# Kernel tuning notes

Measured on AMD Instinct MI355X. Metric: run time of the kernel, lower is better.

Reference implementation:

```python
import jax, jax.numpy as jnp
import numpy as np

DIM = 64  # head dim, init arg
SCALE = DIM ** -0.5

def setup_inputs() -> dict:
    key = jax.random.key(0)
    kq, kk, kv = jax.random.split(key, 3)
    shape = (4, 2048, 8, 64)  # (b, n, h, d)
    q = jax.random.normal(kq, shape, dtype=jnp.float32)
    k = jax.random.normal(kk, shape, dtype=jnp.float32)
    v = jax.random.normal(kv, shape, dtype=jnp.float32)
    return {"q": q, "k": k, "v": v}

def reference(q, k, v):
    # score: [b, h, n_q, n_k] -- matches torch bmm over (b*h) batched [n, d] x [d, n]
    score = jnp.einsum('bqhd,bkhd->bhqk', q, k) * SCALE
    attn = jax.nn.softmax(score, axis=-1)
    # context back to [b, n, h, d] (torch permutes h,b,n,d -> b,n,h,d)
    context = jnp.einsum('bhqk,bkhd->bqhd', attn, v)
    return context
```

## Files before the change

kernel.cpp:

```cpp
#include <hip/hip_runtime.h>

#define B 4
#define N 2048
#define H 8
#define D 64
#define HD 512
#define PLS 72

typedef _Float16 half8 __attribute__((ext_vector_type(8)));
typedef _Float16 half4 __attribute__((ext_vector_type(4)));
typedef float float4_ __attribute__((ext_vector_type(4)));

__global__ void prep_kernel(const float* __restrict__ K, const float* __restrict__ V,
                            _Float16* __restrict__ Kf, _Float16* __restrict__ Vtr) {
    __shared__ _Float16 tile[64][PLS];
    const int t = threadIdx.x;
    if (blockIdx.x < 2048) {
        const size_t i = (size_t)blockIdx.x * 256 + t;
        const float4_* p = (const float4_*)(K + i * 8);
        float4_ a = p[0], b = p[1];
        half8 hh;
        #pragma unroll
        for (int j = 0; j < 4; ++j) { hh[j] = (_Float16)a[j]; hh[4 + j] = (_Float16)b[j]; }
        *(half8*)(Kf + i * 8) = hh;
    } else {
        const int bid = blockIdx.x - 2048;
        const int nt = bid & 31, h = (bid >> 5) & 7, b = bid >> 8;
        {
            const int i = t >> 2, c0 = (t & 3) * 16;
            const float* vp = V + (size_t)b * N * HD + (size_t)(nt * 64 + i) * HD + h * D + c0;
            #pragma unroll
            for (int j = 0; j < 4; ++j) {
                float4_ a = *(const float4_*)(vp + j * 4);
                #pragma unroll
                for (int c = 0; c < 4; ++c) tile[i][c0 + j * 4 + c] = (_Float16)a[c];
            }
        }
        __syncthreads();
        {
            const int d = t >> 2, n0 = (t & 3) * 16;
            half8 lo, hi;
            #pragma unroll
            for (int j = 0; j < 8; ++j) { lo[j] = tile[n0 + j][d]; hi[j] = tile[n0 + 8 + j][d]; }
            _Float16* op = Vtr + ((size_t)(b * H + h) * D + d) * N + nt * 64 + n0;
            *(half8*)op = lo;
            *(half8*)(op + 8) = hi;
        }
    }
}

__device__ __forceinline__ void stage_k(const _Float16* __restrict__ Kbh, int keybase,
                                        _Float16* kb, int wave, int lane) {
    const int rsub = lane >> 3, slot = lane & 7;
    #pragma unroll
    for (int i = 0; i < 2; ++i) {
        const int row = wave * 16 + i * 8 + rsub;
        const int c = slot ^ (row & 7);
        __builtin_amdgcn_global_load_lds(
            (const __attribute__((address_space(1))) void*)(Kbh + (size_t)(keybase + row) * HD + c * 8),
            (__attribute__((address_space(3))) void*)(kb + (wave * 16 + i * 8) * 64), 16, 0, 0);
    }
}
__device__ __forceinline__ void stage_v(const _Float16* __restrict__ Vbh, int keybase,
                                        _Float16* vb, int wave, int lane) {
    const int rsub = lane >> 3, slot = lane & 7;
    #pragma unroll
    for (int i = 0; i < 2; ++i) {
        const int row = wave * 16 + i * 8 + rsub;
        const int c = slot ^ (row & 7);
        __builtin_amdgcn_global_load_lds(
            (const __attribute__((address_space(1))) void*)(Vbh + (size_t)row * N + keybase + c * 8),
            (__attribute__((address_space(3))) void*)(vb + (wave * 16 + i * 8) * 64), 16, 0, 0);
    }
}

__device__ __forceinline__ void do_st4(const _Float16* Kt, const half8 qf[4][2],
                                       float lsum[4], _Float16* PwW, int m, int quad) {
    half8 kfr[4][2];
    #pragma unroll
    for (int blk = 0; blk < 4; ++blk) {
        const int key = blk * 16 + m;
        kfr[blk][0] = *(const half8*)(Kt + key * 64 + ((quad ^ (m & 7)) * 8));
        kfr[blk][1] = *(const half8*)(Kt + key * 64 + (((4 + quad) ^ (m & 7)) * 8));
    }
    #pragma unroll
    for (int blk = 0; blk < 4; ++blk) {
        #pragma unroll
        for (int u = 0; u < 4; ++u) {
            float4_ acc = {};
            acc = __builtin_amdgcn_mfma_f32_16x16x32_f16(kfr[blk][0], qf[u][0], acc, 0, 0, 0);
            acc = __builtin_amdgcn_mfma_f32_16x16x32_f16(kfr[blk][1], qf[u][1], acc, 0, 0, 0);
            half4 pk;
            #pragma unroll
            for (int r = 0; r < 4; ++r) {
                float p = __builtin_amdgcn_exp2f(acc[r]);
                lsum[u] += p;
                pk[r] = (_Float16)p;
            }
            *(half4*)(PwW + (u * 16 + m) * 64 + ((blk * 16 + quad * 4) ^ ((m & 7) << 3))) = pk;
        }
    }
}

__device__ __forceinline__ void load_af4(half8 af[4][2], const _Float16* PwW, int m, int quad) {
    #pragma unroll
    for (int u = 0; u < 4; ++u)
        #pragma unroll
        for (int ks = 0; ks < 2; ++ks)
            af[u][ks] = *(const half8*)(PwW + (u * 16 + m) * 64
                                        + ((ks * 32 + quad * 8) ^ ((m & 7) << 3)));
}

__device__ __forceinline__ void do_pv4(const _Float16* Vtile, const half8 af[4][2],
                                       float4_ o[4][4], int m, int quad) {
    #pragma unroll
    for (int ks = 0; ks < 2; ++ks)
        #pragma unroll
        for (int db = 0; db < 4; ++db) {
            half8 bf = *(const half8*)(Vtile + (db * 16 + m) * 64
                                       + ((((ks << 2) + quad) ^ (m & 7)) * 8));
            #pragma unroll
            for (int u = 0; u < 4; ++u)
                o[u][db] = __builtin_amdgcn_mfma_f32_16x16x32_f16(af[u][ks], bf, o[u][db], 0, 0, 0);
        }
}

__global__ __launch_bounds__(256, 2)
void fattn6_kernel(const float* __restrict__ Q, const _Float16* __restrict__ Kf,
                   const _Float16* __restrict__ Vt, float* __restrict__ O0,
                   float* __restrict__ O1, float* __restrict__ L0, float* __restrict__ L1)
{
    __shared__ __align__(16) _Float16 Kb[2][64 * 64];
    __shared__ __align__(16) _Float16 Vb[2][64 * 64];
    __shared__ __align__(16) _Float16 Pw[4][64 * 64];

    const int tid  = threadIdx.x;
    const int wave = tid >> 6;
    const int lane = tid & 63;
    const int m    = lane & 15;
    const int quad = lane >> 4;

    const int s  = blockIdx.x & 1;
    const int qt = blockIdx.x >> 1;
    const int h  = blockIdx.y;
    const int b  = blockIdx.z;
    const int q_base = qt * 256 + wave * 64;
    const int kofs = s * (N / 2);
    const int NIT = (N / 2) / 64;

    const size_t bh_q = (size_t)b * N * HD + (size_t)h * D;
    const _Float16* Kbh = Kf + bh_q;
    const _Float16* Vbh = Vt + (size_t)(b * H + h) * D * N;
    _Float16* PwW = Pw[wave];

    const float SC = 0.125f * 1.4426950408889634f;
    half8 qf[4][2];
    #pragma unroll
    for (int u = 0; u < 4; ++u) {
        const float* qp = Q + bh_q + (size_t)(q_base + u * 16 + m) * HD + quad * 8;
        float4_ a0 = *(const float4_*)qp,        a1 = *(const float4_*)(qp + 4);
        float4_ b0 = *(const float4_*)(qp + 32), b1 = *(const float4_*)(qp + 36);
        #pragma unroll
        for (int jj = 0; jj < 4; ++jj) {
            qf[u][0][jj] = (_Float16)(a0[jj] * SC); qf[u][0][4 + jj] = (_Float16)(a1[jj] * SC);
            qf[u][1][jj] = (_Float16)(b0[jj] * SC); qf[u][1][4 + jj] = (_Float16)(b1[jj] * SC);
        }
    }

    float4_ o[4][4] = {};
    float lsum[4] = {0.f, 0.f, 0.f, 0.f};

    stage_k(Kbh, kofs, Kb[0], wave, lane);
    __syncthreads();
    stage_k(Kbh, kofs + 64, Kb[1], wave, lane);
    stage_v(Vbh, kofs, Vb[0], wave, lane);
    do_st4(Kb[0], qf, lsum, PwW, m, quad);

    for (int t = 1; t < NIT; ++t) {
        __syncthreads();
        if (t + 1 < NIT)
            stage_k(Kbh, kofs + (t + 1) * 64, Kb[(t + 1) & 1], wave, lane);
        stage_v(Vbh, kofs + t * 64, Vb[t & 1], wave, lane);

        half8 af[4][2];
        load_af4(af, PwW, m, quad);
        do_st4(Kb[t & 1], qf, lsum, PwW, m, quad);
        do_pv4(Vb[(t - 1) & 1], af, o, m, quad);
    }

    __syncthreads();
    {
        half8 af[4][2];
        load_af4(af, PwW, m, quad);
        do_pv4(Vb[(NIT - 1) & 1], af, o, m, quad);
    }

    float lr[4];
    #pragma unroll
    for (int u = 0; u < 4; ++u) {
        float v = lsum[u];
        v += __shfl_xor(v, 16, 64);
        v += __shfl_xor(v, 32, 64);
        lr[u] = v;
    }
    float* Od = s ? O1 : O0;
    float* Ld = s ? L1 : L0;
    if (lane < 16) {
        #pragma unroll
        for (int u = 0; u < 4; ++u)
            Ld[(size_t)(b * H + h) * N + q_base + u * 16 + lane] = lr[u];
    }
    #pragma unroll
    for (int u = 0; u < 4; ++u)
        #pragma unroll
        for (int db = 0; db < 4; ++db)
            #pragma unroll
            for (int r = 0; r < 4; ++r) {
                const int row = q_base + u * 16 + quad * 4 + r;
                Od[bh_q + (size_t)row * HD + db * 16 + m] = o[u][db][r];
            }
}

__global__ void combine_kernel(float* __restrict__ out, const float* __restrict__ O1,
                               const float* __restrict__ L0, const float* __restrict__ L1) {
    const size_t i = ((size_t)blockIdx.x * 256 + threadIdx.x) * 4;
    const int hh = (int)((i >> 6) & 7);
    const int nn = (int)((i >> 9) & 2047);
    const int bb = (int)(i >> 20);
    const size_t qi = ((size_t)(bb * 8 + hh) << 11) | (size_t)nn;
    const float r = 1.0f / (L0[qi] + L1[qi]);
    float4_ a = *(const float4_*)(out + i);
    float4_ c = *(const float4_*)(O1 + i);
    float4_ res;
    #pragma unroll
    for (int j = 0; j < 4; ++j) res[j] = (a[j] + c[j]) * r;
    *(float4_*)(out + i) = res;
}

__device__ __forceinline__ void do_st(const _Float16* Kt, const half8 qf[2][2],
                                      float lsum[2], _Float16* PwW, int m, int quad) {
    #pragma unroll
    for (int blk = 0; blk < 4; ++blk) {
        const int key = blk * 16 + m;
        half8 kf0 = *(const half8*)(Kt + key * 64 + ((quad ^ (m & 7)) * 8));
        half8 kf1 = *(const half8*)(Kt + key * 64 + (((4 + quad) ^ (m & 7)) * 8));
        #pragma unroll
        for (int u = 0; u < 2; ++u) {
            float4_ acc = {};
            acc = __builtin_amdgcn_mfma_f32_16x16x32_f16(kf0, qf[u][0], acc, 0, 0, 0);
            acc = __builtin_amdgcn_mfma_f32_16x16x32_f16(kf1, qf[u][1], acc, 0, 0, 0);
            half4 pk;
            #pragma unroll
            for (int r = 0; r < 4; ++r) {
                float p = __builtin_amdgcn_exp2f(acc[r]);
                lsum[u] += p;
                pk[r] = (_Float16)p;
            }
            *(half4*)(PwW + (u * 16 + m) * 64 + ((blk * 16 + quad * 4) ^ ((m & 7) << 3))) = pk;
        }
    }
}
__device__ __forceinline__ void load_af(half8 af[2][2], const _Float16* PwW, int m, int quad) {
    #pragma unroll
    for (int u = 0; u < 2; ++u)
        #pragma unroll
        for (int ks = 0; ks < 2; ++ks)
            af[u][ks] = *(const half8*)(PwW + (u * 16 + m) * 64
                                        + ((ks * 32 + quad * 8) ^ ((m & 7) << 3)));
}
__device__ __forceinline__ void do_pv(const _Float16* Vtile, const half8 af[2][2],
                                      float4_ o[2][4], int m, int quad) {
    #pragma unroll
    for (int ks = 0; ks < 2; ++ks)
        #pragma unroll
        for (int db = 0; db < 4; ++db) {
            half8 bf = *(const half8*)(Vtile + (db * 16 + m) * 64
                                       + ((((ks << 2) + quad) ^ (m & 7)) * 8));
            #pragma unroll
            for (int u = 0; u < 2; ++u)
                o[u][db] = __builtin_amdgcn_mfma_f32_16x16x32_f16(af[u][ks], bf, o[u][db], 0, 0, 0);
        }
}

__global__ __launch_bounds__(256, 2)
void fattn5_kernel(const float* __restrict__ Q, const _Float16* __restrict__ Kf,
                   const _Float16* __restrict__ Vt, float* __restrict__ Out)
{
    __shared__ __align__(16) _Float16 Kb[2][64 * 64];
    __shared__ __align__(16) _Float16 Vb[2][64 * 64];
    __shared__ __align__(16) _Float16 Pw[4][32 * 64];

    const int tid  = threadIdx.x;
    const int wave = tid >> 6, lane = tid & 63;
    const int m = lane & 15, quad = lane >> 4;
    const int h = blockIdx.y, b = blockIdx.z;
    const int q_base = blockIdx.x * 128 + wave * 32;
    const size_t bh_q = (size_t)b * N * HD + (size_t)h * D;
    const _Float16* Kbh = Kf + bh_q;
    const _Float16* Vbh = Vt + (size_t)(b * H + h) * D * N;
    _Float16* PwW = Pw[wave];
    const float SC = 0.125f * 1.4426950408889634f;
    half8 qf[2][2];
    #pragma unroll
    for (int u = 0; u < 2; ++u) {
        const float* qp = Q + bh_q + (size_t)(q_base + u * 16 + m) * HD + quad * 8;
        float4_ a0 = *(const float4_*)qp,        a1 = *(const float4_*)(qp + 4);
        float4_ b0 = *(const float4_*)(qp + 32), b1 = *(const float4_*)(qp + 36);
        #pragma unroll
        for (int jj = 0; jj < 4; ++jj) {
            qf[u][0][jj] = (_Float16)(a0[jj] * SC); qf[u][0][4 + jj] = (_Float16)(a1[jj] * SC);
            qf[u][1][jj] = (_Float16)(b0[jj] * SC); qf[u][1][4 + jj] = (_Float16)(b1[jj] * SC);
        }
    }
    float4_ o[2][4] = {};
    float lsum[2] = {0.f, 0.f};
    stage_k(Kbh, 0, Kb[0], wave, lane);
    __syncthreads();
    stage_k(Kbh, 64, Kb[1], wave, lane);
    stage_v(Vbh, 0, Vb[0], wave, lane);
    do_st(Kb[0], qf, lsum, PwW, m, quad);
    for (int t = 1; t < 32; ++t) {
        __syncthreads();
        if (t + 1 < 32) stage_k(Kbh, (t + 1) * 64, Kb[(t + 1) & 1], wave, lane);
        stage_v(Vbh, t * 64, Vb[t & 1], wave, lane);
        half8 af[2][2];
        load_af(af, PwW, m, quad);
        do_st(Kb[t & 1], qf, lsum, PwW, m, quad);
        do_pv(Vb[(t - 1) & 1], af, o, m, quad);
    }
    __syncthreads();
    {
        half8 af[2][2];
        load_af(af, PwW, m, quad);
        do_pv(Vb[31 & 1], af, o, m, quad);
    }
    float inv[2];
    #pragma unroll
    for (int u = 0; u < 2; ++u) {
        float v = lsum[u];
        v += __shfl_xor(v, 16, 64);
        v += __shfl_xor(v, 32, 64);
        inv[u] = 1.0f / v;
    }
    #pragma unroll
    for (int u = 0; u < 2; ++u)
        #pragma unroll
        for (int r = 0; r < 4; ++r) {
            const int src = (lane & 48) | (quad * 4 + r);
            const float linv = __shfl(inv[u], src, 64);
            const int row = q_base + u * 16 + quad * 4 + r;
            #pragma unroll
            for (int db = 0; db < 4; ++db)
                Out[bh_q + (size_t)row * HD + db * 16 + m] = o[u][db][r] * linv;
        }
}

__global__ __launch_bounds__(256, 2)
void fattn_fb_kernel(const float* __restrict__ Q, const float* __restrict__ K,
                     const float* __restrict__ V, float* __restrict__ Out)
{
    __shared__ __align__(16) _Float16 Ks[64][PLS];
    __shared__ __align__(16) _Float16 Vts[D][PLS];
    __shared__ __align__(16) _Float16 Pwf[4][16][PLS];
    const int tid = threadIdx.x, wave = tid >> 6, lane = tid & 63;
    const int m = lane & 15, quad = lane >> 4;
    const int q_base = blockIdx.x * 64;
    const size_t bh_off = ((size_t)blockIdx.z * N * H + (size_t)blockIdx.y) * D;
    const float SCALE = 0.125f;
    const int qrow = q_base + wave * 16 + m;
    const float* qp = Q + bh_off + (size_t)qrow * HD + quad * 8;
    half8 qf0, qf1;
    #pragma unroll
    for (int j = 0; j < 8; ++j) qf0[j] = (_Float16)(qp[j] * SCALE);
    #pragma unroll
    for (int j = 0; j < 8; ++j) qf1[j] = (_Float16)(qp[32 + j] * SCALE);
    float4_ o[4] = {};
    float mi[4], li[4];
    #pragma unroll
    for (int r = 0; r < 4; ++r) { mi[r] = -1e30f; li[r] = 0.0f; }
    for (int kt = 0; kt < N; kt += 64) {
        __syncthreads();
        {
            const int key = tid >> 2, c0 = (tid & 3) * 16;
            const float* kp = K + bh_off + (size_t)(kt + key) * HD + c0;
            half8 lo, hi;
            #pragma unroll
            for (int j = 0; j < 8; ++j) lo[j] = (_Float16)kp[j];
            #pragma unroll
            for (int j = 0; j < 8; ++j) hi[j] = (_Float16)kp[8 + j];
            *(half8*)&Ks[key][c0] = lo;
            *(half8*)&Ks[key][c0 + 8] = hi;
        }
        {
            const int c0 = (tid & 15) * 4, k0 = (tid >> 4) * 4;
            const float* vp = V + bh_off + (size_t)(kt + k0) * HD + c0;
            #pragma unroll
            for (int c = 0; c < 4; ++c)
                #pragma unroll
                for (int i = 0; i < 4; ++i)
                    Vts[c0 + c][k0 + i] = (_Float16)vp[i * HD + c];
        }
        __syncthreads();
        float4_ s[4];
        #pragma unroll
        for (int blk = 0; blk < 4; ++blk) {
            const int key = blk * 16 + m;
            half8 kf0 = *(const half8*)&Ks[key][quad * 8];
            half8 kf1 = *(const half8*)&Ks[key][32 + quad * 8];
            float4_ acc = {};
            acc = __builtin_amdgcn_mfma_f32_16x16x32_f16(qf0, kf0, acc, 0, 0, 0);
            acc = __builtin_amdgcn_mfma_f32_16x16x32_f16(qf1, kf1, acc, 0, 0, 0);
            s[blk] = acc;
        }
        float alpha[4];
        #pragma unroll
        for (int r = 0; r < 4; ++r) {
            float v0 = fmaxf(fmaxf(s[0][r], s[1][r]), fmaxf(s[2][r], s[3][r]));
            #pragma unroll
            for (int mask = 1; mask < 16; mask <<= 1) v0 = fmaxf(v0, __shfl_xor(v0, mask, 64));
            float mn = fmaxf(mi[r], v0);
            alpha[r] = __expf(mi[r] - mn);
            mi[r] = mn;
        }
        #pragma unroll
        for (int blk = 0; blk < 4; ++blk)
            #pragma unroll
            for (int r = 0; r < 4; ++r) s[blk][r] = __expf(s[blk][r] - mi[r]);
        #pragma unroll
        for (int r = 0; r < 4; ++r) {
            float tt = s[0][r] + s[1][r] + s[2][r] + s[3][r];
            #pragma unroll
            for (int mask = 1; mask < 16; mask <<= 1) tt += __shfl_xor(tt, mask, 64);
            li[r] = li[r] * alpha[r] + tt;
        }
        #pragma unroll
        for (int d = 0; d < 4; ++d)
            #pragma unroll
            for (int r = 0; r < 4; ++r) o[d][r] *= alpha[r];
        #pragma unroll
        for (int blk = 0; blk < 4; ++blk)
            #pragma unroll
            for (int r = 0; r < 4; ++r)
                Pwf[wave][quad * 4 + r][blk * 16 + m] = (_Float16)s[blk][r];
        #pragma unroll
        for (int ks = 0; ks < 2; ++ks) {
            half8 af = *(const half8*)&Pwf[wave][m][ks * 32 + quad * 8];
            #pragma unroll
            for (int d = 0; d < 4; ++d) {
                half8 bf = *(const half8*)&Vts[d * 16 + m][ks * 32 + quad * 8];
                o[d] = __builtin_amdgcn_mfma_f32_16x16x32_f16(af, bf, o[d], 0, 0, 0);
            }
        }
    }
    #pragma unroll
    for (int d = 0; d < 4; ++d)
        #pragma unroll
        for (int r = 0; r < 4; ++r) {
            const int row = q_base + wave * 16 + quad * 4 + r;
            Out[bh_off + (size_t)row * HD + d * 16 + m] = o[d][r] / li[r];
        }
}

extern "C" void kernel_launch(void* const* d_in, const int* in_sizes, int n_in,
                              void* d_out, int out_size, void* d_ws, size_t ws_size,
                              hipStream_t stream) {
    const float* q = (const float*)d_in[0];
    const float* k = (const float*)d_in[1];
    const float* v = (const float*)d_in[2];
    float* out = (float*)d_out;

    const size_t nelem = (size_t)B * N * H * D;
    const size_t nrows = (size_t)B * H * N;
    const size_t need5 = 2 * nelem * sizeof(_Float16);
    const size_t need6 = need5 + nelem * sizeof(float) + 2 * nrows * sizeof(float);

    if (ws_size >= need6) {
        _Float16* Kf  = (_Float16*)d_ws;
        _Float16* Vtr = Kf + nelem;
        float* O1 = (float*)(Vtr + nelem);
        float* L0 = O1 + nelem;
        float* L1 = L0 + nrows;
        prep_kernel<<<dim3(3072), 256, 0, stream>>>(k, v, Kf, Vtr);
        fattn6_kernel<<<dim3(16, H, B), 256, 0, stream>>>(q, Kf, Vtr, out, O1, L0, L1);
        combine_kernel<<<dim3(4096), 256, 0, stream>>>(out, O1, L0, L1);
    } else if (ws_size >= need5) {
        _Float16* Kf  = (_Float16*)d_ws;
        _Float16* Vtr = Kf + nelem;
        prep_kernel<<<dim3(3072), 256, 0, stream>>>(k, v, Kf, Vtr);
        fattn5_kernel<<<dim3(16, H, B), 256, 0, stream>>>(q, Kf, Vtr, out);
    } else {
        fattn_fb_kernel<<<dim3(N / 64, H, B), 256, 0, stream>>>(q, k, v, out);
    }
}
```

Before: 144.2 us.

## Split keys four ways with fp16 partials and single-buffered smaller LDS

Raises the key-dimension split from two to four, so the attention grid has twice as many blocks. LDS use drops from double-buffered K/V plus 64-wide P to single buffers plus a 32-wide P tile, and launch bounds move to four blocks per CU. Partial outputs are now stored in fp16 and reduced across four splits by a new combine kernel. This targets higher occupancy and better CU fill, at the cost of losing the load/compute overlap of double buffering, adding two barriers per iteration, more combine traffic, and fp16 rounding of the partial sums.

Result: slower. 352.9 us (+144.7%).

```diff
diff --git a/kernel.cpp b/kernel.cpp
--- a/kernel.cpp
+++ b/kernel.cpp
@@ -6,6 +6,9 @@
 #define D 64
 #define HD 512
 #define PLS 72
+#define NELEM ((size_t)B * N * H * D)
+#define NROWS ((size_t)B * H * N)
+#define SPLIT 4
 
 typedef _Float16 half8 __attribute__((ext_vector_type(8)));
 typedef _Float16 half4 __attribute__((ext_vector_type(4)));
@@ -74,65 +77,14 @@
     }
 }
 
-__device__ __forceinline__ void do_st4(const _Float16* Kt, const half8 qf[4][2],
-                                       float lsum[4], _Float16* PwW, int m, int quad) {
-    half8 kfr[4][2];
-    #pragma unroll
-    for (int blk = 0; blk < 4; ++blk) {
-        const int key = blk * 16 + m;
-        kfr[blk][0] = *(const half8*)(Kt + key * 64 + ((quad ^ (m & 7)) * 8));
-        kfr[blk][1] = *(const half8*)(Kt + key * 64 + (((4 + quad) ^ (m & 7)) * 8));
-    }
-    #pragma unroll
-    for (int blk = 0; blk < 4; ++blk) {
-        #pragma unroll
-        for (int u = 0; u < 4; ++u) {
-            float4_ acc = {};
-            acc = __builtin_amdgcn_mfma_f32_16x16x32_f16(kfr[blk][0], qf[u][0], acc, 0, 0, 0);
-            acc = __builtin_amdgcn_mfma_f32_16x16x32_f16(kfr[blk][1], qf[u][1], acc, 0, 0, 0);
-            half4 pk;
-            #pragma unroll
-            for (int r = 0; r < 4; ++r) {
-                float p = __builtin_amdgcn_exp2f(acc[r]);
-                lsum[u] += p;
-                pk[r] = (_Float16)p;
-            }
-            *(half4*)(PwW + (u * 16 + m) * 64 + ((blk * 16 + quad * 4) ^ ((m & 7) << 3))) = pk;
-        }
-    }
-}
-
-__device__ __forceinline__ void load_af4(half8 af[4][2], const _Float16* PwW, int m, int quad) {
-    #pragma unroll
-    for (int u = 0; u < 4; ++u)
-        #pragma unroll
-        for (int ks = 0; ks < 2; ++ks)
-            af[u][ks] = *(const half8*)(PwW + (u * 16 + m) * 64
-                                        + ((ks * 32 + quad * 8) ^ ((m & 7) << 3)));
-}
-
-__device__ __forceinline__ void do_pv4(const _Float16* Vtile, const half8 af[4][2],
-                                       float4_ o[4][4], int m, int quad) {
-    #pragma unroll
-    for (int ks = 0; ks < 2; ++ks)
-        #pragma unroll
-        for (int db = 0; db < 4; ++db) {
-            half8 bf = *(const half8*)(Vtile + (db * 16 + m) * 64
-                                       + ((((ks << 2) + quad) ^ (m & 7)) * 8));
-            #pragma unroll
-            for (int u = 0; u < 4; ++u)
-                o[u][db] = __builtin_amdgcn_mfma_f32_16x16x32_f16(af[u][ks], bf, o[u][db], 0, 0, 0);
-        }
-}
-
-__global__ __launch_bounds__(256, 2)
-void fattn6_kernel(const float* __restrict__ Q, const _Float16* __restrict__ Kf,
-                   const _Float16* __restrict__ Vt, float* __restrict__ O0,
-                   float* __restrict__ O1, float* __restrict__ L0, float* __restrict__ L1)
+__global__ __launch_bounds__(256, 4)
+void fattn7_kernel(const float* __restrict__ Q, const _Float16* __restrict__ Kf,
+                   const _Float16* __restrict__ Vt, _Float16* __restrict__ Op,
+                   float* __restrict__ Lp)
 {
-    __shared__ __align__(16) _Float16 Kb[2][64 * 64];
-    __shared__ __align__(16) _Float16 Vb[2][64 * 64];
-    __shared__ __align__(16) _Float16 Pw[4][64 * 64];
+    __shared__ __align__(16) _Float16 Kb[64 * 64];
+    __shared__ __align__(16) _Float16 Vb[64 * 64];
+    __shared__ __align__(16) _Float16 Pw[4][64 * 32];
 
     const int tid  = threadIdx.x;
     const int wave = tid >> 6;
@@ -140,13 +92,13 @@
     const int m    = lane & 15;
     const int quad = lane >> 4;
 
-    const int s  = blockIdx.x & 1;
-    const int qt = blockIdx.x >> 1;
+    const int s  = blockIdx.x & 3;
+    const int qt = blockIdx.x >> 2;
     const int h  = blockIdx.y;
     const int b  = blockIdx.z;
     const int q_base = qt * 256 + wave * 64;
-    const int kofs = s * (N / 2);
-    const int NIT = (N / 2) / 64;
+    const int kofs = s * (N / SPLIT);
+    const int NIT = (N / SPLIT) / 64;
 
     const size_t bh_q = (size_t)b * N * HD + (size_t)h * D;
     const _Float16* Kbh = Kf + bh_q;
@@ -170,29 +122,51 @@
     float4_ o[4][4] = {};
     float lsum[4] = {0.f, 0.f, 0.f, 0.f};
 
-    stage_k(Kbh, kofs, Kb[0], wave, lane);
-    __syncthreads();
-    stage_k(Kbh, kofs + 64, Kb[1], wave, lane);
-    stage_v(Vbh, kofs, Vb[0], wave, lane);
-    do_st4(Kb[0], qf, lsum, PwW, m, quad);
-
-    for (int t = 1; t < NIT; ++t) {
-        __syncthreads();
-        if (t + 1 < NIT)
-            stage_k(Kbh, kofs + (t + 1) * 64, Kb[(t + 1) & 1], wave, lane);
-        stage_v(Vbh, kofs + t * 64, Vb[t & 1], wave, lane);
-
-        half8 af[4][2];
-        load_af4(af, PwW, m, quad);
-        do_st4(Kb[t & 1], qf, lsum, PwW, m, quad);
-        do_pv4(Vb[(t - 1) & 1], af, o, m, quad);
-    }
-
-    __syncthreads();
-    {
-        half8 af[4][2];
-        load_af4(af, PwW, m, quad);
-        do_pv4(Vb[(NIT - 1) & 1], af, o, m, quad);
+    for (int t = 0; t < NIT; ++t) {
+        __syncthreads();
+        stage_k(Kbh, kofs + t * 64, Kb, wave, lane);
+        stage_v(Vbh, kofs + t * 64, Vb, wave, lane);
+        __syncthreads();
+
+        #pragma unroll
+        for (int sp = 0; sp < 2; ++sp) {
+            #pragma unroll
+            for (int bb = 0; bb < 2; ++bb) {
+                const int key = (sp * 2 + bb) * 16 + m;
+                half8 kf0 = *(const half8*)(Kb + key * 64 + ((quad ^ (m & 7)) * 8));
+                half8 kf1 = *(const half8*)(Kb + key * 64 + (((4 + quad) ^ (m & 7)) * 8));
+                #pragma unroll
+                for (int u = 0; u < 4; ++u) {
+                    float4_ acc = {};
+                    acc = __builtin_amdgcn_mfma_f32_16x16x32_f16(kf0, qf[u][0], acc, 0, 0, 0);
+                    acc = __builtin_amdgcn_mfma_f32_16x16x32_f16(kf1, qf[u][1], acc, 0, 0, 0);
+                    half4 pk;
+                    #pragma unroll
+                    for (int r = 0; r < 4; ++r) {
+                        float p = __builtin_amdgcn_exp2f(acc[r]);
+                        lsum[u] += p;
+                        pk[r] = (_Float16)p;
+                    }
+                    *(half4*)(PwW + (u * 16 + m) * 32 + (((bb * 4 + quad) ^ (m & 7)) * 4)) = pk;
+                }
+            }
+
+            half8 af[4];
+            #pragma unroll
+            for (int u = 0; u < 4; ++u) {
+                half4 lo = *(const half4*)(PwW + (u * 16 + m) * 32 + (((2 * quad) ^ (m & 7)) * 4));
+                half4 hi = *(const half4*)(PwW + (u * 16 + m) * 32 + (((2 * quad + 1) ^ (m & 7)) * 4));
+                #pragma unroll
+                for (int jj = 0; jj < 4; ++jj) { af[u][jj] = lo[jj]; af[u][4 + jj] = hi[jj]; }
+            }
+            #pragma unroll
+            for (int db = 0; db < 4; ++db) {
+                half8 bf = *(const half8*)(Vb + (db * 16 + m) * 64 + (((sp * 4 + quad) ^ (m & 7)) * 8));
+                #pragma unroll
+                for (int u = 0; u < 4; ++u)
+                    o[u][db] = __builtin_amdgcn_mfma_f32_16x16x32_f16(af[u], bf, o[u][db], 0, 0, 0);
+            }
+        }
     }
 
     float lr[4];
@@ -203,13 +177,13 @@
         v += __shfl_xor(v, 32, 64);
         lr[u] = v;
     }
-    float* Od = s ? O1 : O0;
-    float* Ld = s ? L1 : L0;
+    float* Ld = Lp + (size_t)s * NROWS;
     if (lane < 16) {
         #pragma unroll
         for (int u = 0; u < 4; ++u)
             Ld[(size_t)(b * H + h) * N + q_base + u * 16 + lane] = lr[u];
     }
+    _Float16* Od = Op + (size_t)s * NELEM;
     #pragma unroll
     for (int u = 0; u < 4; ++u)
         #pragma unroll
@@ -217,24 +191,30 @@
             #pragma unroll
             for (int r = 0; r < 4; ++r) {
                 const int row = q_base + u * 16 + quad * 4 + r;
-                Od[bh_q + (size_t)row * HD + db * 16 + m] = o[u][db][r];
-            }
-}
-
-__global__ void combine_kernel(float* __restrict__ out, const float* __restrict__ O1,
-                               const float* __restrict__ L0, const float* __restrict__ L1) {
-    const size_t i = ((size_t)blockIdx.x * 256 + threadIdx.x) * 4;
+                Od[bh_q + (size_t)row * HD + db * 16 + m] = (_Float16)o[u][db][r];
+            }
+}
+
+__global__ void combine4_kernel(float* __restrict__ out, const _Float16* __restrict__ Op,
+                                const float* __restrict__ Lp) {
+    const size_t i = ((size_t)blockIdx.x * 256 + threadIdx.x) * 8;
     const int hh = (int)((i >> 6) & 7);
     const int nn = (int)((i >> 9) & 2047);
     const int bb = (int)(i >> 20);
     const size_t qi = ((size_t)(bb * 8 + hh) << 11) | (size_t)nn;
-    const float r = 1.0f / (L0[qi] + L1[qi]);
-    float4_ a = *(const float4_*)(out + i);
-    float4_ c = *(const float4_*)(O1 + i);
-    float4_ res;
-    #pragma unroll
-    for (int j = 0; j < 4; ++j) res[j] = (a[j] + c[j]) * r;
-    *(float4_*)(out + i) = res;
+    const float r = 1.0f / (Lp[qi] + Lp[NROWS + qi] + Lp[2 * NROWS + qi] + Lp[3 * NROWS + qi]);
+    float acc[8] = {};
+    #pragma unroll
+    for (int s = 0; s < 4; ++s) {
+        half8 hv = *(const half8*)(Op + (size_t)s * NELEM + i);
+        #pragma unroll
+        for (int j = 0; j < 8; ++j) acc[j] += (float)hv[j];
+    }
+    float4_ r0, r1;
+    #pragma unroll
+    for (int j = 0; j < 4; ++j) { r0[j] = acc[j] * r; r1[j] = acc[4 + j] * r; }
+    *(float4_*)(out + i) = r0;
+    *(float4_*)(out + i + 4) = r1;
 }
 
 __device__ __forceinline__ void do_st(const _Float16* Kt, const half8 qf[2][2],
@@ -286,9 +266,9 @@
 void fattn5_kernel(const float* __restrict__ Q, const _Float16* __restrict__ Kf,
                    const _Float16* __restrict__ Vt, float* __restrict__ Out)
 {
-    __shared__ __align__(16) _Float16 Kb[2][64 * 64];
-    __shared__ __align__(16) _Float16 Vb[2][64 * 64];
-    __shared__ __align__(16) _Float16 Pw[4][32 * 64];
+    __shared__ __align__(16) _Float16 Kb2[2][64 * 64];
+    __shared__ __align__(16) _Float16 Vb2[2][64 * 64];
+    __shared__ __align__(16) _Float16 Pw2[4][32 * 64];
 
     const int tid  = threadIdx.x;
     const int wave = tid >> 6, lane = tid & 63;
@@ -298,7 +278,7 @@
     const size_t bh_q = (size_t)b * N * HD + (size_t)h * D;
     const _Float16* Kbh = Kf + bh_q;
     const _Float16* Vbh = Vt + (size_t)(b * H + h) * D * N;
-    _Float16* PwW = Pw[wave];
+    _Float16* PwW = Pw2[wave];
     const float SC = 0.125f * 1.4426950408889634f;
     half8 qf[2][2];
     #pragma unroll
@@ -314,25 +294,25 @@
     }
     float4_ o[2][4] = {};
     float lsum[2] = {0.f, 0.f};
-    stage_k(Kbh, 0, Kb[0], wave, lane);
+    stage_k(Kbh, 0, Kb2[0], wave, lane);
     __syncthreads();
-    stage_k(Kbh, 64, Kb[1], wave, lane);
-    stage_v(Vbh, 0, Vb[0], wave, lane);
-    do_st(Kb[0], qf, lsum, PwW, m, quad);
+    stage_k(Kbh, 64, Kb2[1], wave, lane);
+    stage_v(Vbh, 0, Vb2[0], wave, lane);
+    do_st(Kb2[0], qf, lsum, PwW, m, quad);
     for (int t = 1; t < 32; ++t) {
         __syncthreads();
-        if (t + 1 < 32) stage_k(Kbh, (t + 1) * 64, Kb[(t + 1) & 1], wave, lane);
-        stage_v(Vbh, t * 64, Vb[t & 1], wave, lane);
+        if (t + 1 < 32) stage_k(Kbh, (t + 1) * 64, Kb2[(t + 1) & 1], wave, lane);
+        stage_v(Vbh, t * 64, Vb2[t & 1], wave, lane);
         half8 af[2][2];
         load_af(af, PwW, m, quad);
-        do_st(Kb[t & 1], qf, lsum, PwW, m, quad);
-        do_pv(Vb[(t - 1) & 1], af, o, m, quad);
+        do_st(Kb2[t & 1], qf, lsum, PwW, m, quad);
+        do_pv(Vb2[(t - 1) & 1], af, o, m, quad);
     }
     __syncthreads();
     {
         half8 af[2][2];
         load_af(af, PwW, m, quad);
-        do_pv(Vb[31 & 1], af, o, m, quad);
+        do_pv(Vb2[1], af, o, m, quad);
     }
     float inv[2];
     #pragma unroll
@@ -469,23 +449,21 @@
     const float* v = (const float*)d_in[2];
     float* out = (float*)d_out;
 
-    const size_t nelem = (size_t)B * N * H * D;
-    const size_t nrows = (size_t)B * H * N;
-    const size_t need5 = 2 * nelem * sizeof(_Float16);
-    const size_t need6 = need5 + nelem * sizeof(float) + 2 * nrows * sizeof(float);
-
-    if (ws_size >= need6) {
+    const size_t need5 = 2 * NELEM * sizeof(_Float16);
+    const size_t need7 = need5 + SPLIT * NELEM * sizeof(_Float16)
+                               + SPLIT * NROWS * sizeof(float);
+
+    if (ws_size >= need7) {
         _Float16* Kf  = (_Float16*)d_ws;
-        _Float16* Vtr = Kf + nelem;
-        float* O1 = (float*)(Vtr + nelem);
-        float* L0 = O1 + nelem;
-        float* L1 = L0 + nrows;
+        _Float16* Vtr = Kf + NELEM;
+        _Float16* Op  = Vtr + NELEM;
+        float* Lp = (float*)(Op + SPLIT * NELEM);
         prep_kernel<<<dim3(3072), 256, 0, stream>>>(k, v, Kf, Vtr);
-        fattn6_kernel<<<dim3(16, H, B), 256, 0, stream>>>(q, Kf, Vtr, out, O1, L0, L1);
-        combine_kernel<<<dim3(4096), 256, 0, stream>>>(out, O1, L0, L1);
+        fattn7_kernel<<<dim3((N / 256) * SPLIT, H, B), 256, 0, stream>>>(q, Kf, Vtr, Op, Lp);
+        combine4_kernel<<<dim3(NELEM / 8 / 256), 256, 0, stream>>>(out, Op, Lp);
     } else if (ws_size >= need5) {
         _Float16* Kf  = (_Float16*)d_ws;
-        _Float16* Vtr = Kf + nelem;
+        _Float16* Vtr = Kf + NELEM;
         prep_kernel<<<dim3(3072), 256, 0, stream>>>(k, v, Kf, Vtr);
         fattn5_kernel<<<dim3(16, H, B), 256, 0, stream>>>(q, Kf, Vtr, out);
     } else {
```
